# Optimization experiments

Measured on AMD Instinct MI355X. Metric: run time of the kernel, lower is better.

Reference implementation:

```python
import jax, jax.numpy as jnp
import numpy as np

SOS = 0
MAX_LENGTH = 64

N_LATENTS = 256
N_CHARACTERS = 128
N_HIDDENS = 1024
BATCH = 4096


def setup_inputs() -> dict:
    key = jax.random.key(0)
    ks = jax.random.split(key, 16)
    H, L, C = N_HIDDENS, N_LATENTS, N_CHARACTERS
    s = 0.02
    return {
        "z": jax.random.normal(ks[0], (BATCH, L), dtype=jnp.float32),
        "embed_w": jax.random.normal(ks[1], (C, H), dtype=jnp.float32) * s,
        "z2h_w": jax.random.normal(ks[2], (H, L), dtype=jnp.float32) * s,
        "z2h_b": jnp.zeros((H,), dtype=jnp.float32),
        "w_ih0": jax.random.normal(ks[3], (3 * H, H + L), dtype=jnp.float32) * s,
        "w_hh0": jax.random.normal(ks[4], (3 * H, H), dtype=jnp.float32) * s,
        "b_ih0": jnp.zeros((3 * H,), dtype=jnp.float32),
        "b_hh0": jnp.zeros((3 * H,), dtype=jnp.float32),
        "w_ih1": jax.random.normal(ks[5], (3 * H, H), dtype=jnp.float32) * s,
        "w_hh1": jax.random.normal(ks[6], (3 * H, H), dtype=jnp.float32) * s,
        "b_ih1": jnp.zeros((3 * H,), dtype=jnp.float32),
        "b_hh1": jnp.zeros((3 * H,), dtype=jnp.float32),
        "h2o_w": jax.random.normal(ks[7], (C, H + L), dtype=jnp.float32) * s,
        "h2o_b": jnp.zeros((C,), dtype=jnp.float32),
    }


def _gru_cell(x, h, w_ih, w_hh, b_ih, b_hh):
    # PyTorch GRUCell math. x: [B, I], h: [B, H]
    gi = x @ w_ih.T + b_ih  # [B, 3H]
    gh = h @ w_hh.T + b_hh  # [B, 3H]
    i_r, i_z, i_n = jnp.split(gi, 3, axis=1)
    h_r, h_z, h_n = jnp.split(gh, 3, axis=1)
    r = jax.nn.sigmoid(i_r + h_r)
    zg = jax.nn.sigmoid(i_z + h_z)
    n = jnp.tanh(i_n + r * h_n)
    return (1.0 - zg) * n + zg * h


def reference(z, embed_w, z2h_w, z2h_b,
              w_ih0, w_hh0, b_ih0, b_hh0,
              w_ih1, w_hh1, b_ih1, b_hh1,
              h2o_w, h2o_b):
    batch = z.shape[0]
    h0 = z @ z2h_w.T + z2h_b  # [B, H], replicated across both GRU layers

    def step(carry, _):
        c_in, h1, h2 = carry
        e = embed_w[c_in]                      # [B, H] embedding lookup
        e = e * jax.nn.sigmoid(e)              # swish
        x = jnp.concatenate([e, z], axis=1)    # [B, H+L]
        h1 = _gru_cell(x, h1, w_ih0, w_hh0, b_ih0, b_hh0)
        h2 = _gru_cell(h1, h2, w_ih1, w_hh1, b_ih1, b_hh1)
        out = jnp.concatenate([h2, z], axis=1) @ h2o_w.T + h2o_b  # [B, C]
        # argmax(log_softmax(out)) == argmax(out)
        sample = jnp.argmax(out, axis=1).astype(jnp.int32)
        return (sample, h1, h2), out

    c0 = jnp.full((batch,), SOS, dtype=jnp.int32)
    _, outs = jax.lax.scan(step, (c0, h0, h0), None, length=MAX_LENGTH)
    return jnp.transpose(outs, (1, 0, 2))  # [B, T, C]
```

## Files before the change

### kernel.cpp

```cpp
#include <hip/hip_runtime.h>
#include <hip/hip_bf16.h>
#include <stdint.h>
#include <stddef.h>

#define B_   4096
#define H_   1024
#define L_   256
#define C_   128
#define T_   64
#define H3_  3072

typedef unsigned short u16;
typedef __attribute__((ext_vector_type(8))) short bf16x8;
typedef __attribute__((ext_vector_type(4))) float f32x4;

typedef const void __attribute__((address_space(1)))* as1_cvp;
typedef void __attribute__((address_space(3)))* as3_vp;

__device__ __forceinline__ void gl2lds16(const void* g, void* l) {
  __builtin_amdgcn_global_load_lds((as1_cvp)g, (as3_vp)l, 16, 0, 0);
}

__device__ __forceinline__ float bf2f(u16 u) {
  union { float f; unsigned int i; } x; x.i = ((unsigned int)u) << 16; return x.f;
}
__device__ __forceinline__ u16 f2bf(float f) {
  union { float f; unsigned int i; } x; x.f = f;
  unsigned int r = x.i + 0x7fffu + ((x.i >> 16) & 1u);
  return (u16)(r >> 16);
}
__device__ __forceinline__ float sigm(float x) { return 1.f / (1.f + __expf(-x)); }
__device__ __forceinline__ float tanh_fast(float x) {
  float e = __expf(2.f * x); return 1.f - 2.f / (e + 1.f);
}

template<int OUT_MODE>
__device__ __forceinline__ void gemm_tile_body(
    u16* As, u16* Ws,
    const u16* __restrict__ A, int lda,
    const u16* __restrict__ W, int ldw,
    const float* __restrict__ bias,
    void* __restrict__ C0p, void* __restrict__ C1p, int ldc, int K,
    int m0, int n0)
{
  const int tid  = threadIdx.x;
  const int wave = tid >> 6, lane = tid & 63;
  const int wm = (wave >> 1) * 64, wn = (wave & 1) * 64;
  const int lrow = lane & 15, lq = lane >> 4;
  const int arow = wave * 8 + (lane >> 3);
  const int acol = (lane & 7) * 8;

  f32x4 acc[4][4] = {};

  const u16* Ag = A + (size_t)m0 * lda;
  const u16* Wg = W + (size_t)n0 * ldw;

  for (int k0 = 0; k0 < K; k0 += 64) {
    __syncthreads();
    #pragma unroll
    for (int rd = 0; rd < 4; rd++) {
      gl2lds16(Ag + (size_t)(rd * 32 + arow) * lda + (k0 + acol), As + rd * 2048 + wave * 512);
      gl2lds16(Wg + (size_t)(rd * 32 + arow) * ldw + (k0 + acol), Ws + rd * 2048 + wave * 512);
    }
    __syncthreads();
    #pragma unroll
    for (int kk = 0; kk < 64; kk += 32) {
      bf16x8 af[4], bw[4];
      #pragma unroll
      for (int i = 0; i < 4; i++)
        af[i] = *(const bf16x8*)&As[(wm + i * 16 + lrow) * 64 + kk + lq * 8];
      #pragma unroll
      for (int j = 0; j < 4; j++)
        bw[j] = *(const bf16x8*)&Ws[(wn + j * 16 + lrow) * 64 + kk + lq * 8];
      #pragma unroll
      for (int i = 0; i < 4; i++)
        #pragma unroll
        for (int j = 0; j < 4; j++)
          acc[i][j] = __builtin_amdgcn_mfma_f32_16x16x32_bf16(af[i], bw[j], acc[i][j], 0, 0, 0);
    }
  }

  #pragma unroll
  for (int j = 0; j < 4; j++) {
    const int col = n0 + wn + j * 16 + lrow;
    const float bv = bias ? bias[col] : 0.f;
    #pragma unroll
    for (int i = 0; i < 4; i++) {
      #pragma unroll
      for (int r = 0; r < 4; r++) {
        const int row = m0 + wm + i * 16 + lq * 4 + r;
        float v = acc[i][j][r] + bv;
        if (OUT_MODE == 0) {
          ((float*)C0p)[(size_t)row * ldc + col] = v;
        } else if (OUT_MODE == 1) {
          ((u16*)C0p)[(size_t)row * ldc + col] = f2bf(v);
        } else {
          u16 hv = f2bf(v);
          ((u16*)C0p)[(size_t)row * ldc + col] = hv;
          ((u16*)C1p)[(size_t)row * ldc + col] = hv;
        }
      }
    }
  }
}

template<int OUT_MODE>
__global__ __launch_bounds__(256) void gemm_bt(
    const u16* __restrict__ A, int lda,
    const u16* __restrict__ W, int ldw,
    const float* __restrict__ bias,
    void* __restrict__ C0p, void* __restrict__ C1p, int ldc, int K)
{
  __shared__ __align__(16) u16 As[128 * 64];
  __shared__ __align__(16) u16 Ws[128 * 64];
  gemm_tile_body<OUT_MODE>(As, Ws, A, lda, W, ldw, bias, C0p, C1p, ldc, K,
                           blockIdx.y * 128, blockIdx.x * 128);
}

__device__ __forceinline__ void out_body(
    u16* As, u16* Ws, int ob,
    const u16* __restrict__ h2, const u16* __restrict__ Wo,
    const float* __restrict__ Oz, float* __restrict__ outp,
    int* __restrict__ cnew, int t)
{
  const int tid = threadIdx.x, wave = tid >> 6, lane = tid & 63;
  const int b0 = ob * 64;
  const int lrow = lane & 15, lq = lane >> 4;
  const int arow = wave * 8 + (lane >> 3);
  const int acol = (lane & 7) * 8;
  f32x4 acc[8] = {};

  for (int k0 = 0; k0 < H_; k0 += 64) {
    __syncthreads();
    #pragma unroll
    for (int rd = 0; rd < 2; rd++)
      gl2lds16(h2 + (size_t)(b0 + rd * 32 + arow) * H_ + k0 + acol, As + rd * 2048 + wave * 512);
    #pragma unroll
    for (int rd = 0; rd < 4; rd++)
      gl2lds16(Wo + (size_t)(rd * 32 + arow) * H_ + k0 + acol, Ws + rd * 2048 + wave * 512);
    __syncthreads();
    #pragma unroll
    for (int kk = 0; kk < 64; kk += 32) {
      bf16x8 af = *(const bf16x8*)&As[(wave * 16 + lrow) * 64 + kk + lq * 8];
      #pragma unroll
      for (int j = 0; j < 8; j++) {
        bf16x8 bw = *(const bf16x8*)&Ws[(j * 16 + lrow) * 64 + kk + lq * 8];
        acc[j] = __builtin_amdgcn_mfma_f32_16x16x32_bf16(af, bw, acc[j], 0, 0, 0);
      }
    }
  }

  #pragma unroll
  for (int r = 0; r < 4; r++) {
    const int row = b0 + wave * 16 + lq * 4 + r;
    float mv = -3.4e38f; int mi = 0;
    #pragma unroll
    for (int j = 0; j < 8; j++) {
      const int col = j * 16 + lrow;
      float v = acc[j][r] + Oz[(size_t)row * C_ + col];
      outp[(size_t)row * (T_ * C_) + t * C_ + col] = v;
      if (v > mv) { mv = v; mi = col; }
    }
    #pragma unroll
    for (int off = 1; off < 16; off <<= 1) {
      float ov = __shfl_xor(mv, off);
      int   oi = __shfl_xor(mi, off);
      if (ov > mv || (ov == mv && oi < mi)) { mv = ov; mi = oi; }
    }
    if (lrow == 0) cnew[row] = mi;
  }
}

__global__ __launch_bounds__(256) void out_k(
    const u16* __restrict__ h2cur, const u16* __restrict__ Wo,
    const float* __restrict__ Oz, float* __restrict__ outp,
    int* __restrict__ cbuf, int t)
{
  __shared__ __align__(16) u16 As[64 * 64];
  __shared__ __align__(16) u16 Ws[128 * 64];
  out_body(As, Ws, blockIdx.x, h2cur, Wo, Oz, outp, cbuf, t);
}


__device__ __forceinline__ void stage256(const u16* Ag, const u16* Wg, int k0,
                                         u16* bA, u16* bW) {
  const int tid = threadIdx.x;
  const int wave = tid >> 6, lane = tid & 63;
  const int r64 = wave * 8 + (lane >> 3);
  const int cSw = (((lane & 7) ^ ((lane >> 5) << 1)) << 3);
  #pragma unroll
  for (int rd = 0; rd < 4; rd++)
    gl2lds16(Ag + (size_t)(rd * 64 + r64) * H_ + k0 + cSw, bA + rd * 4096 + wave * 512);
  #pragma unroll
  for (int rd = 0; rd < 3; rd++)
    gl2lds16(Wg + (size_t)(rd * 1024 + r64) * H_ + k0 + cSw, bW + rd * 4096 + wave * 512);
}

template<bool PH2>
__device__ __forceinline__ void tile_mfma(const u16* bA, const u16* bW,
                                          f32x4 acc[3][2][4], f32x4 accN[2][4]) {
  const int tid = threadIdx.x;
  const int wave = tid >> 6, lane = tid & 63;
  const int wmh = wave >> 1, wj = wave & 1;
  const int lrow = lane & 15, lq = lane >> 4;
  const int rsw = ((lrow >> 2) & 1) << 4;
  #pragma unroll
  for (int kk = 0; kk < 64; kk += 32) {
    const int csw = (kk + lq * 8) ^ rsw;
    bf16x8 af[4];
    #pragma unroll
    for (int i = 0; i < 4; i++)
      af[i] = *(const bf16x8*)&bA[(wmh * 64 + i * 16 + lrow) * 64 + csw];
    #pragma unroll
    for (int g = 0; g < 3; g++) {
      #pragma unroll
      for (int u = 0; u < 2; u++) {
        bf16x8 bw = *(const bf16x8*)&bW[(g * 64 + wj * 32 + u * 16 + lrow) * 64 + csw];
        #pragma unroll
        for (int i = 0; i < 4; i++) {
          if (PH2 && g == 2)
            accN[u][i] = __builtin_amdgcn_mfma_f32_16x16x32_bf16(af[i], bw, accN[u][i], 0, 0, 0);
          else
            acc[g][u][i] = __builtin_amdgcn_mfma_f32_16x16x32_bf16(af[i], bw, acc[g][u][i], 0, 0, 0);
        }
      }
    }
  }
}

template<int NT1, int NT2>
__device__ __forceinline__ void kloop_pipe(
    u16* As, u16* Ws,
    const u16* A1g, const u16* W1g,
    const u16* A2g, const u16* W2g,
    f32x4 acc[3][2][4], f32x4 accN[2][4])
{
  constexpr int NT = NT1 + NT2;
  stage256(A1g, W1g, 0, As, Ws);
  if (NT1 > 1) stage256(A1g, W1g, 64, As + 16384, Ws + 12288);
  else         stage256(A2g, W2g, 0,  As + 16384, Ws + 12288);

  #pragma unroll 2
  for (int v = 0; v < NT1; v++) {
    u16* bA = (v & 1) ? As + 16384 : As;
    u16* bW = (v & 1) ? Ws + 12288 : Ws;
    if (v + 1 < NT) asm volatile("s_waitcnt vmcnt(7)" ::: "memory");
    else            asm volatile("s_waitcnt vmcnt(0)" ::: "memory");
    __builtin_amdgcn_sched_barrier(0);
    __builtin_amdgcn_s_barrier();
    __builtin_amdgcn_sched_barrier(0);
    __builtin_amdgcn_s_setprio(1);
    tile_mfma<false>(bA, bW, acc, accN);
    __builtin_amdgcn_s_setprio(0);
    __builtin_amdgcn_sched_barrier(0);
    __builtin_amdgcn_s_barrier();
    __builtin_amdgcn_sched_barrier(0);
    const int w = v + 2;
    if (w < NT) {
      const u16* Av = (w < NT1) ? A1g : A2g;
      const u16* Wv = (w < NT1) ? W1g : W2g;
      const int k0 = ((w < NT1) ? w : w - NT1) * 64;
      stage256(Av, Wv, k0, bA, bW);
    }
  }
  #pragma unroll 2
  for (int v = NT1; v < NT; v++) {
    u16* bA = (v & 1) ? As + 16384 : As;
    u16* bW = (v & 1) ? Ws + 12288 : Ws;
    if (v + 1 < NT) asm volatile("s_waitcnt vmcnt(7)" ::: "memory");
    else            asm volatile("s_waitcnt vmcnt(0)" ::: "memory");
    __builtin_amdgcn_sched_barrier(0);
    __builtin_amdgcn_s_barrier();
    __builtin_amdgcn_sched_barrier(0);
    __builtin_amdgcn_s_setprio(1);
    tile_mfma<true>(bA, bW, acc, accN);
    __builtin_amdgcn_s_setprio(0);
    __builtin_amdgcn_sched_barrier(0);
    __builtin_amdgcn_s_barrier();
    __builtin_amdgcn_sched_barrier(0);
    const int w = v + 2;
    if (w < NT)
      stage256(A2g, W2g, (w - NT1) * 64, bA, bW);
  }
}

__global__ __launch_bounds__(512, 2) void gru0_256(
    const u16* __restrict__ h1old, const u16* __restrict__ whh0,
    const float* __restrict__ b_hh0, const int* __restrict__ cbuf,
    const u16* __restrict__ Egi, const u16* __restrict__ Gz,
    u16* __restrict__ h1new)
{
  __shared__ __align__(16) u16 As[2 * 16384];
  __shared__ __align__(16) u16 Ws[2 * 12288];
  const int bid = blockIdx.x;
  const int xcd = bid & 7, k = bid >> 3;
  const int jt = xcd * 2 + (k & 1);
  const int m  = k >> 1;
  const int m0 = m * 256, j0 = jt * 64;

  f32x4 acc[3][2][4] = {};
  f32x4 accN[2][4] = {};
  kloop_pipe<16, 0>(As, Ws,
                    h1old + (size_t)m0 * H_, whh0 + (size_t)j0 * H_,
                    h1old + (size_t)m0 * H_, whh0 + (size_t)j0 * H_,
                    acc, accN);

  const int tid = threadIdx.x, wave = tid >> 6, lane = tid & 63;
  const int wmh = wave >> 1, wj = wave & 1;
  const int lrow = lane & 15, lq = lane >> 4;

  #pragma unroll
  for (int u = 0; u < 2; u++) {
    const int j = j0 + wj * 32 + u * 16 + lrow;
    const float bR = b_hh0[j];
    const float bZ = b_hh0[H_ + j];
    const float bN = b_hh0[2 * H_ + j];
    #pragma unroll
    for (int i = 0; i < 4; i++) {
      #pragma unroll
      for (int rr = 0; rr < 4; rr++) {
        const int row = m0 + wmh * 64 + i * 16 + lq * 4 + rr;
        const size_t eb = (size_t)cbuf[row] * H3_ + j;
        const size_t gb = (size_t)row * H3_ + j;
        float r  = sigm(bf2f(Egi[eb])           + bf2f(Gz[gb])           + acc[0][u][i][rr] + bR);
        float zg = sigm(bf2f(Egi[eb + H_])      + bf2f(Gz[gb + H_])      + acc[1][u][i][rr] + bZ);
        float nn = tanh_fast(bf2f(Egi[eb + 2 * H_]) + bf2f(Gz[gb + 2 * H_])
                             + r * (acc[2][u][i][rr] + bN));
        float hold = bf2f(h1old[(size_t)row * H_ + j]);
        h1new[(size_t)row * H_ + j] = f2bf((1.f - zg) * nn + zg * hold);
      }
    }
  }
}

__global__ __launch_bounds__(512, 2) void gru1_256(
    const u16* __restrict__ h1, const u16* __restrict__ h2old,
    const u16* __restrict__ wih1, const u16* __restrict__ whh1,
    const float* __restrict__ b_ih1, const float* __restrict__ b_hh1,
    u16* __restrict__ h2new)
{
  __shared__ __align__(16) u16 As[2 * 16384];
  __shared__ __align__(16) u16 Ws[2 * 12288];
  const int bid = blockIdx.x;
  const int xcd = bid & 7, k = bid >> 3;
  const int jt = xcd * 2 + (k & 1);
  const int m  = k >> 1;
  const int m0 = m * 256, j0 = jt * 64;

  f32x4 acc[3][2][4] = {};
  f32x4 accN[2][4] = {};
  kloop_pipe<16, 16>(As, Ws,
                     h1    + (size_t)m0 * H_, wih1 + (size_t)j0 * H_,
                     h2old + (size_t)m0 * H_, whh1 + (size_t)j0 * H_,
                     acc, accN);

  const int tid = threadIdx.x, wave = tid >> 6, lane = tid & 63;
  const int wmh = wave >> 1, wj = wave & 1;
  const int lrow = lane & 15, lq = lane >> 4;

  #pragma unroll
  for (int u = 0; u < 2; u++) {
    const int j = j0 + wj * 32 + u * 16 + lrow;
    const float bR  = b_ih1[j] + b_hh1[j];
    const float bZ  = b_ih1[H_ + j] + b_hh1[H_ + j];
    const float bNi = b_ih1[2 * H_ + j];
    const float bNh = b_hh1[2 * H_ + j];
    #pragma unroll
    for (int i = 0; i < 4; i++) {
      #pragma unroll
      for (int rr = 0; rr < 4; rr++) {
        const int row = m0 + wmh * 64 + i * 16 + lq * 4 + rr;
        float r  = sigm(acc[0][u][i][rr] + bR);
        float zg = sigm(acc[1][u][i][rr] + bZ);
        float nn = tanh_fast(acc[2][u][i][rr] + bNi + r * (accN[u][i][rr] + bNh));
        float hold = bf2f(h2old[(size_t)row * H_ + j]);
        h2new[(size_t)row * H_ + j] = f2bf((1.f - zg) * nn + zg * hold);
      }
    }
  }
}

__global__ __launch_bounds__(256) void conv_bf16_k(const float* __restrict__ s, u16* __restrict__ d, int n) {
  int i = blockIdx.x * 256 + threadIdx.x;
  if (i < n) d[i] = f2bf(s[i]);
}
__global__ __launch_bounds__(256) void conv_split_k(const float* __restrict__ s, u16* __restrict__ dA,
                                                    u16* __restrict__ dZ, int rows) {
  int i = blockIdx.x * 256 + threadIdx.x;
  if (i >= rows * 1280) return;
  int rr = i / 1280, col = i - rr * 1280;
  float v = s[i];
  if (col < 1024) dA[(size_t)rr * 1024 + col] = f2bf(v);
  else            dZ[(size_t)rr * 256 + (col - 1024)] = f2bf(v);
}
__global__ __launch_bounds__(256) void conv_swish_k(const float* __restrict__ s, u16* __restrict__ d, int n) {
  int i = blockIdx.x * 256 + threadIdx.x;
  if (i < n) { float e = s[i]; d[i] = f2bf(e * sigm(e)); }
}

static inline char* wsal(char*& p, size_t bytes) {
  char* r = p; p += (bytes + 255) & ~(size_t)255; return r;
}

extern "C" void kernel_launch(void* const* d_in, const int* in_sizes, int n_in,
                              void* d_out, int out_size, void* d_ws, size_t ws_size,
                              hipStream_t stream) {
  const float* z       = (const float*)d_in[0];
  const float* embed_w = (const float*)d_in[1];
  const float* z2h_w   = (const float*)d_in[2];
  const float* z2h_b   = (const float*)d_in[3];
  const float* w_ih0   = (const float*)d_in[4];
  const float* w_hh0   = (const float*)d_in[5];
  const float* b_ih0   = (const float*)d_in[6];
  const float* b_hh0   = (const float*)d_in[7];
  const float* w_ih1   = (const float*)d_in[8];
  const float* w_hh1   = (const float*)d_in[9];
  const float* b_ih1   = (const float*)d_in[10];
  const float* b_hh1   = (const float*)d_in[11];
  const float* h2o_w   = (const float*)d_in[12];
  const float* h2o_b   = (const float*)d_in[13];
  float* outp = (float*)d_out;

  char* p = (char*)d_ws;
  u16* whh0  = (u16*)wsal(p, (size_t)H3_ * H_ * 2);
  u16* wih1  = (u16*)wsal(p, (size_t)H3_ * H_ * 2);
  u16* whh1  = (u16*)wsal(p, (size_t)H3_ * H_ * 2);
  u16* wih0a = (u16*)wsal(p, (size_t)H3_ * H_ * 2);
  u16* wih0z = (u16*)wsal(p, (size_t)H3_ * L_ * 2);
  u16* h2oa  = (u16*)wsal(p, (size_t)C_ * H_ * 2);
  u16* h2oz  = (u16*)wsal(p, (size_t)C_ * L_ * 2);
  u16* z2hb  = (u16*)wsal(p, (size_t)H_ * L_ * 2);
  u16* zb    = (u16*)wsal(p, (size_t)B_ * L_ * 2);
  u16* swe   = (u16*)wsal(p, (size_t)C_ * H_ * 2);
  u16* EgiB  = (u16*)wsal(p, (size_t)C_ * H3_ * 2);
  u16* Gz    = (u16*)wsal(p, (size_t)B_ * H3_ * 2);
  float* Oz  = (float*)wsal(p, (size_t)B_ * C_ * 4);
  u16* h1a   = (u16*)wsal(p, (size_t)B_ * H_ * 2);
  u16* h1b   = (u16*)wsal(p, (size_t)B_ * H_ * 2);
  u16* h2a   = (u16*)wsal(p, (size_t)B_ * H_ * 2);
  u16* h2b   = (u16*)wsal(p, (size_t)B_ * H_ * 2);
  int* cbuf  = (int*)wsal(p, (size_t)B_ * 4);

  conv_bf16_k<<<(B_*L_ + 255)/256, 256, 0, stream>>>(z, zb, B_*L_);
  conv_bf16_k<<<(H_*L_ + 255)/256, 256, 0, stream>>>(z2h_w, z2hb, H_*L_);
  conv_bf16_k<<<(H3_*H_ + 255)/256, 256, 0, stream>>>(w_hh0, whh0, H3_*H_);
  conv_bf16_k<<<(H3_*H_ + 255)/256, 256, 0, stream>>>(w_ih1, wih1, H3_*H_);
  conv_bf16_k<<<(H3_*H_ + 255)/256, 256, 0, stream>>>(w_hh1, whh1, H3_*H_);
  conv_split_k<<<(H3_*1280 + 255)/256, 256, 0, stream>>>(w_ih0, wih0a, wih0z, H3_);
  conv_split_k<<<(C_*1280 + 255)/256, 256, 0, stream>>>(h2o_w, h2oa, h2oz, C_);
  conv_swish_k<<<(C_*H_ + 255)/256, 256, 0, stream>>>(embed_w, swe, C_*H_);
  hipMemsetAsync(cbuf, 0, B_ * sizeof(int), stream);

  gemm_bt<2><<<dim3(H_/128, B_/128), 256, 0, stream>>>(zb, L_, z2hb, L_, z2h_b, h1a, h2a, H_, L_);
  gemm_bt<1><<<dim3(H3_/128, 1), 256, 0, stream>>>(swe, H_, wih0a, H_, b_ih0, EgiB, nullptr, H3_, H_);
  gemm_bt<1><<<dim3(H3_/128, B_/128), 256, 0, stream>>>(zb, L_, wih0z, L_, nullptr, Gz, nullptr, H3_, L_);
  gemm_bt<0><<<dim3(1, B_/128), 256, 0, stream>>>(zb, L_, h2oz, L_, h2o_b, Oz, nullptr, C_, L_);

  for (int t = 0; t < T_; t++) {
    const u16* h2cur = (t & 1) ? h2b : h2a;
    u16*       h2nxt = (t & 1) ? h2a : h2b;
    const u16* h1cur = (t & 1) ? h1b : h1a;
    u16*       h1nxt = (t & 1) ? h1a : h1b;
    if (t > 0)
      out_k<<<64, 256, 0, stream>>>(h2cur, h2oa, Oz, outp, cbuf, t - 1);
    gru0_256<<<256, 512, 0, stream>>>(h1cur, whh0, b_hh0, cbuf, EgiB, Gz, h1nxt);
    gru1_256<<<256, 512, 0, stream>>>(h1nxt, h2cur, wih1, whh1, b_ih1, b_hh1, h2nxt);
  }
  out_k<<<64, 256, 0, stream>>>(h2a, h2oa, Oz, outp, cbuf, T_ - 1);
}
```

Measured before the change: 7.824 ms.

## Interleave LDS reads, MFMA and staged global loads in three phases per tile

Replaces the double-buffered GEMM k-loop in both GRU kernels with a schedule that splits each 64-wide k-tile into three phases. Each phase reads its fragments from LDS, issues part of the next tiles' global-to-LDS loads (W for the next tile, A halves for two tiles ahead), then runs its MFMA batch. A is now triple-buffered and W double-buffered, raising LDS to 144KB per block. The aim is to spread memory traffic across the MFMA work and shorten exposed load latency, at the cost of more barriers and explicit lgkmcnt waits per tile.

New measurement: 7.143 ms. -8.7%, faster.

```diff
diff --git a/kernel.cpp b/kernel.cpp
--- a/kernel.cpp
+++ b/kernel.cpp
@@ -182,105 +182,204 @@
 }
 
 
-__device__ __forceinline__ void stage256(const u16* Ag, const u16* Wg, int k0,
-                                         u16* bA, u16* bW) {
-  const int tid = threadIdx.x;
-  const int wave = tid >> 6, lane = tid & 63;
+#define A_TSZ 16384
+#define W_TSZ 12288
+
+__device__ __forceinline__ void stageA_lo(const u16* Ag, int k0, u16* bA) {
+  const int tid = threadIdx.x, wave = tid >> 6, lane = tid & 63;
+  const int r64 = wave * 8 + (lane >> 3);
+  const int cSw = (((lane & 7) ^ ((lane >> 5) << 1)) << 3);
+  gl2lds16(Ag + (size_t)(r64) * H_ + k0 + cSw, bA + wave * 512);
+  gl2lds16(Ag + (size_t)(64 + r64) * H_ + k0 + cSw, bA + 4096 + wave * 512);
+}
+__device__ __forceinline__ void stageA_hi(const u16* Ag, int k0, u16* bA) {
+  const int tid = threadIdx.x, wave = tid >> 6, lane = tid & 63;
+  const int r64 = wave * 8 + (lane >> 3);
+  const int cSw = (((lane & 7) ^ ((lane >> 5) << 1)) << 3);
+  gl2lds16(Ag + (size_t)(128 + r64) * H_ + k0 + cSw, bA + 8192 + wave * 512);
+  gl2lds16(Ag + (size_t)(192 + r64) * H_ + k0 + cSw, bA + 12288 + wave * 512);
+}
+__device__ __forceinline__ void stageW(const u16* Wg, int k0, u16* bW) {
+  const int tid = threadIdx.x, wave = tid >> 6, lane = tid & 63;
   const int r64 = wave * 8 + (lane >> 3);
   const int cSw = (((lane & 7) ^ ((lane >> 5) << 1)) << 3);
   #pragma unroll
-  for (int rd = 0; rd < 4; rd++)
-    gl2lds16(Ag + (size_t)(rd * 64 + r64) * H_ + k0 + cSw, bA + rd * 4096 + wave * 512);
-  #pragma unroll
   for (int rd = 0; rd < 3; rd++)
     gl2lds16(Wg + (size_t)(rd * 1024 + r64) * H_ + k0 + cSw, bW + rd * 4096 + wave * 512);
 }
 
-template<bool PH2>
-__device__ __forceinline__ void tile_mfma(const u16* bA, const u16* bW,
-                                          f32x4 acc[3][2][4], f32x4 accN[2][4]) {
-  const int tid = threadIdx.x;
-  const int wave = tid >> 6, lane = tid & 63;
+template<int PHASE>
+__device__ __forceinline__ void phase_reads(const u16* bA, const u16* bW,
+    bf16x8 af0[4], bf16x8 af1[4], bf16x8 bwv[2][2])
+{
+  const int tid = threadIdx.x, wave = tid >> 6, lane = tid & 63;
   const int wmh = wave >> 1, wj = wave & 1;
   const int lrow = lane & 15, lq = lane >> 4;
   const int rsw = ((lrow >> 2) & 1) << 4;
-  #pragma unroll
-  for (int kk = 0; kk < 64; kk += 32) {
-    const int csw = (kk + lq * 8) ^ rsw;
-    bf16x8 af[4];
+  const int c0 = (lq * 8) ^ rsw;
+  const int c1 = (32 + lq * 8) ^ rsw;
+  if (PHASE == 0) {
     #pragma unroll
     for (int i = 0; i < 4; i++)
-      af[i] = *(const bf16x8*)&bA[(wmh * 64 + i * 16 + lrow) * 64 + csw];
-    #pragma unroll
-    for (int g = 0; g < 3; g++) {
-      #pragma unroll
-      for (int u = 0; u < 2; u++) {
-        bf16x8 bw = *(const bf16x8*)&bW[(g * 64 + wj * 32 + u * 16 + lrow) * 64 + csw];
-        #pragma unroll
-        for (int i = 0; i < 4; i++) {
-          if (PH2 && g == 2)
-            accN[u][i] = __builtin_amdgcn_mfma_f32_16x16x32_bf16(af[i], bw, accN[u][i], 0, 0, 0);
-          else
-            acc[g][u][i] = __builtin_amdgcn_mfma_f32_16x16x32_bf16(af[i], bw, acc[g][u][i], 0, 0, 0);
-        }
-      }
-    }
-  }
-}
-
-template<int NT1, int NT2>
-__device__ __forceinline__ void kloop_pipe(
-    u16* As, u16* Ws,
-    const u16* A1g, const u16* W1g,
-    const u16* A2g, const u16* W2g,
+      af0[i] = *(const bf16x8*)&bA[(wmh * 64 + i * 16 + lrow) * 64 + c0];
+    #pragma unroll
+    for (int u = 0; u < 2; u++) {
+      bwv[0][u] = *(const bf16x8*)&bW[(wj * 32 + u * 16 + lrow) * 64 + c0];
+      bwv[1][u] = *(const bf16x8*)&bW[(64 + wj * 32 + u * 16 + lrow) * 64 + c0];
+    }
+  } else if (PHASE == 1) {
+    #pragma unroll
+    for (int i = 0; i < 4; i++)
+      af1[i] = *(const bf16x8*)&bA[(wmh * 64 + i * 16 + lrow) * 64 + c1];
+    #pragma unroll
+    for (int u = 0; u < 2; u++) {
+      bwv[0][u] = *(const bf16x8*)&bW[(128 + wj * 32 + u * 16 + lrow) * 64 + c0];
+      bwv[1][u] = *(const bf16x8*)&bW[(wj * 32 + u * 16 + lrow) * 64 + c1];
+    }
+  } else {
+    #pragma unroll
+    for (int u = 0; u < 2; u++) {
+      bwv[0][u] = *(const bf16x8*)&bW[(64 + wj * 32 + u * 16 + lrow) * 64 + c1];
+      bwv[1][u] = *(const bf16x8*)&bW[(128 + wj * 32 + u * 16 + lrow) * 64 + c1];
+    }
+  }
+}
+
+template<int PHASE, bool PH2v>
+__device__ __forceinline__ void phase_fma(const bf16x8 bwv[2][2],
+    const bf16x8 af0[4], const bf16x8 af1[4],
     f32x4 acc[3][2][4], f32x4 accN[2][4])
 {
+  if (PHASE == 0) {
+    #pragma unroll
+    for (int u = 0; u < 2; u++)
+      #pragma unroll
+      for (int i = 0; i < 4; i++) {
+        acc[0][u][i] = __builtin_amdgcn_mfma_f32_16x16x32_bf16(af0[i], bwv[0][u], acc[0][u][i], 0, 0, 0);
+        acc[1][u][i] = __builtin_amdgcn_mfma_f32_16x16x32_bf16(af0[i], bwv[1][u], acc[1][u][i], 0, 0, 0);
+      }
+  } else if (PHASE == 1) {
+    #pragma unroll
+    for (int u = 0; u < 2; u++)
+      #pragma unroll
+      for (int i = 0; i < 4; i++) {
+        if (PH2v)
+          accN[u][i] = __builtin_amdgcn_mfma_f32_16x16x32_bf16(af0[i], bwv[0][u], accN[u][i], 0, 0, 0);
+        else
+          acc[2][u][i] = __builtin_amdgcn_mfma_f32_16x16x32_bf16(af0[i], bwv[0][u], acc[2][u][i], 0, 0, 0);
+        acc[0][u][i] = __builtin_amdgcn_mfma_f32_16x16x32_bf16(af1[i], bwv[1][u], acc[0][u][i], 0, 0, 0);
+      }
+  } else {
+    #pragma unroll
+    for (int u = 0; u < 2; u++)
+      #pragma unroll
+      for (int i = 0; i < 4; i++) {
+        acc[1][u][i] = __builtin_amdgcn_mfma_f32_16x16x32_bf16(af1[i], bwv[0][u], acc[1][u][i], 0, 0, 0);
+        if (PH2v)
+          accN[u][i] = __builtin_amdgcn_mfma_f32_16x16x32_bf16(af1[i], bwv[1][u], accN[u][i], 0, 0, 0);
+        else
+          acc[2][u][i] = __builtin_amdgcn_mfma_f32_16x16x32_bf16(af1[i], bwv[1][u], acc[2][u][i], 0, 0, 0);
+      }
+  }
+}
+
+template<int NT1, int NT2, bool PH2v>
+__device__ __forceinline__ void tile8(
+    int v, u16* aC, u16* wC, u16* wN, u16* aN2,
+    const u16* A1g, const u16* W1g, const u16* A2g, const u16* W2g,
+    f32x4 acc[3][2][4], f32x4 accN[2][4])
+{
   constexpr int NT = NT1 + NT2;
-  stage256(A1g, W1g, 0, As, Ws);
-  if (NT1 > 1) stage256(A1g, W1g, 64, As + 16384, Ws + 12288);
-  else         stage256(A2g, W2g, 0,  As + 16384, Ws + 12288);
-
-  #pragma unroll 2
-  for (int v = 0; v < NT1; v++) {
-    u16* bA = (v & 1) ? As + 16384 : As;
-    u16* bW = (v & 1) ? Ws + 12288 : Ws;
-    if (v + 1 < NT) asm volatile("s_waitcnt vmcnt(7)" ::: "memory");
-    else            asm volatile("s_waitcnt vmcnt(0)" ::: "memory");
-    __builtin_amdgcn_sched_barrier(0);
-    __builtin_amdgcn_s_barrier();
-    __builtin_amdgcn_sched_barrier(0);
-    __builtin_amdgcn_s_setprio(1);
-    tile_mfma<false>(bA, bW, acc, accN);
-    __builtin_amdgcn_s_setprio(0);
-    __builtin_amdgcn_sched_barrier(0);
-    __builtin_amdgcn_s_barrier();
-    __builtin_amdgcn_sched_barrier(0);
+  if (v + 1 < NT) asm volatile("s_waitcnt vmcnt(4)" ::: "memory");
+  else            asm volatile("s_waitcnt vmcnt(0)" ::: "memory");
+  __builtin_amdgcn_sched_barrier(0);
+  __builtin_amdgcn_s_barrier();
+  __builtin_amdgcn_sched_barrier(0);
+
+  bf16x8 af0[4], af1[4], bwv[2][2];
+
+  phase_reads<0>(aC, wC, af0, af1, bwv);
+  {
+    const int w = v + 1;
+    if (w < NT) {
+      const u16* Wg = (w < NT1) ? W1g : W2g;
+      stageW(Wg, ((w < NT1) ? w : w - NT1) * 64, wN);
+    }
+  }
+  asm volatile("s_waitcnt lgkmcnt(0)" ::: "memory");
+  __builtin_amdgcn_sched_barrier(0);
+  __builtin_amdgcn_s_setprio(1);
+  phase_fma<0, PH2v>(bwv, af0, af1, acc, accN);
+  __builtin_amdgcn_s_setprio(0);
+  __builtin_amdgcn_sched_barrier(0);
+  __builtin_amdgcn_s_barrier();
+  __builtin_amdgcn_sched_barrier(0);
+
+  phase_reads<1>(aC, wC, af0, af1, bwv);
+  {
     const int w = v + 2;
     if (w < NT) {
-      const u16* Av = (w < NT1) ? A1g : A2g;
-      const u16* Wv = (w < NT1) ? W1g : W2g;
-      const int k0 = ((w < NT1) ? w : w - NT1) * 64;
-      stage256(Av, Wv, k0, bA, bW);
-    }
-  }
-  #pragma unroll 2
+      const u16* Ag = (w < NT1) ? A1g : A2g;
+      stageA_lo(Ag, ((w < NT1) ? w : w - NT1) * 64, aN2);
+    }
+  }
+  asm volatile("s_waitcnt lgkmcnt(0)" ::: "memory");
+  __builtin_amdgcn_sched_barrier(0);
+  __builtin_amdgcn_s_setprio(1);
+  phase_fma<1, PH2v>(bwv, af0, af1, acc, accN);
+  __builtin_amdgcn_s_setprio(0);
+  __builtin_amdgcn_sched_barrier(0);
+  __builtin_amdgcn_s_barrier();
+  __builtin_amdgcn_sched_barrier(0);
+
+  phase_reads<2>(aC, wC, af0, af1, bwv);
+  {
+    const int w = v + 2;
+    if (w < NT) {
+      const u16* Ag = (w < NT1) ? A1g : A2g;
+      stageA_hi(Ag, ((w < NT1) ? w : w - NT1) * 64, aN2);
+    }
+  }
+  asm volatile("s_waitcnt lgkmcnt(0)" ::: "memory");
+  __builtin_amdgcn_sched_barrier(0);
+  __builtin_amdgcn_s_setprio(1);
+  phase_fma<2, PH2v>(bwv, af0, af1, acc, accN);
+  __builtin_amdgcn_s_setprio(0);
+  __builtin_amdgcn_sched_barrier(0);
+}
+
+template<int NT1, int NT2>
+__device__ __forceinline__ void kloop8(
+    u16* As, u16* Ws,
+    const u16* A1g, const u16* W1g, const u16* A2g, const u16* W2g,
+    f32x4 acc[3][2][4], f32x4 accN[2][4])
+{
+  constexpr int NT = NT1 + NT2;
+  u16* aB0 = As; u16* aB1 = As + A_TSZ; u16* aB2 = As + 2 * A_TSZ;
+  u16* wB0 = Ws; u16* wB1 = Ws + W_TSZ;
+
+  stageA_lo(A1g, 0, aB0); stageA_hi(A1g, 0, aB0);
+  stageW(W1g, 0, wB0);
+  if (NT > 1) {
+    const u16* Ag = (1 < NT1) ? A1g : A2g;
+    const int k0 = (1 < NT1) ? 64 : 0;
+    stageA_lo(Ag, k0, aB1); stageA_hi(Ag, k0, aB1);
+  }
+
+  u16* aC = aB0; u16* aN1 = aB1; u16* aN2 = aB2;
+  u16* wC = wB0; u16* wN = wB1;
+
+  #pragma unroll 1
+  for (int v = 0; v < NT1; v++) {
+    tile8<NT1, NT2, false>(v, aC, wC, wN, aN2, A1g, W1g, A2g, W2g, acc, accN);
+    u16* t = aC; aC = aN1; aN1 = aN2; aN2 = t;
+    u16* tw = wC; wC = wN; wN = tw;
+  }
+  #pragma unroll 1
   for (int v = NT1; v < NT; v++) {
-    u16* bA = (v & 1) ? As + 16384 : As;
-    u16* bW = (v & 1) ? Ws + 12288 : Ws;
-    if (v + 1 < NT) asm volatile("s_waitcnt vmcnt(7)" ::: "memory");
-    else            asm volatile("s_waitcnt vmcnt(0)" ::: "memory");
-    __builtin_amdgcn_sched_barrier(0);
-    __builtin_amdgcn_s_barrier();
-    __builtin_amdgcn_sched_barrier(0);
-    __builtin_amdgcn_s_setprio(1);
-    tile_mfma<true>(bA, bW, acc, accN);
-    __builtin_amdgcn_s_setprio(0);
-    __builtin_amdgcn_sched_barrier(0);
-    __builtin_amdgcn_s_barrier();
-    __builtin_amdgcn_sched_barrier(0);
-    const int w = v + 2;
-    if (w < NT)
-      stage256(A2g, W2g, (w - NT1) * 64, bA, bW);
+    tile8<NT1, NT2, true>(v, aC, wC, wN, aN2, A1g, W1g, A2g, W2g, acc, accN);
+    u16* t = aC; aC = aN1; aN1 = aN2; aN2 = t;
+    u16* tw = wC; wC = wN; wN = tw;
   }
 }
 
@@ -290,8 +389,8 @@
     const u16* __restrict__ Egi, const u16* __restrict__ Gz,
     u16* __restrict__ h1new)
 {
-  __shared__ __align__(16) u16 As[2 * 16384];
-  __shared__ __align__(16) u16 Ws[2 * 12288];
+  __shared__ __align__(16) u16 As[3 * A_TSZ];
+  __shared__ __align__(16) u16 Ws[2 * W_TSZ];
   const int bid = blockIdx.x;
   const int xcd = bid & 7, k = bid >> 3;
   const int jt = xcd * 2 + (k & 1);
@@ -300,10 +399,10 @@
 
   f32x4 acc[3][2][4] = {};
   f32x4 accN[2][4] = {};
-  kloop_pipe<16, 0>(As, Ws,
-                    h1old + (size_t)m0 * H_, whh0 + (size_t)j0 * H_,
-                    h1old + (size_t)m0 * H_, whh0 + (size_t)j0 * H_,
-                    acc, accN);
+  kloop8<16, 0>(As, Ws,
+                h1old + (size_t)m0 * H_, whh0 + (size_t)j0 * H_,
+                h1old + (size_t)m0 * H_, whh0 + (size_t)j0 * H_,
+                acc, accN);
 
   const int tid = threadIdx.x, wave = tid >> 6, lane = tid & 63;
   const int wmh = wave >> 1, wj = wave & 1;
@@ -339,8 +438,8 @@
     const float* __restrict__ b_ih1, const float* __restrict__ b_hh1,
     u16* __restrict__ h2new)
 {
-  __shared__ __align__(16) u16 As[2 * 16384];
-  __shared__ __align__(16) u16 Ws[2 * 12288];
+  __shared__ __align__(16) u16 As[3 * A_TSZ];
+  __shared__ __align__(16) u16 Ws[2 * W_TSZ];
   const int bid = blockIdx.x;
   const int xcd = bid & 7, k = bid >> 3;
   const int jt = xcd * 2 + (k & 1);
@@ -349,10 +448,10 @@
 
   f32x4 acc[3][2][4] = {};
   f32x4 accN[2][4] = {};
-  kloop_pipe<16, 16>(As, Ws,
-                     h1    + (size_t)m0 * H_, wih1 + (size_t)j0 * H_,
-                     h2old + (size_t)m0 * H_, whh1 + (size_t)j0 * H_,
-                     acc, accN);
+  kloop8<16, 16>(As, Ws,
+                 h1    + (size_t)m0 * H_, wih1 + (size_t)j0 * H_,
+                 h2old + (size_t)m0 * H_, whh1 + (size_t)j0 * H_,
+                 acc, accN);
 
   const int tid = threadIdx.x, wave = tid >> 6, lane = tid & 63;
   const int wmh = wave >> 1, wj = wave & 1;
```
